# Kernel optimization log

Hardware: AMD Instinct MI355X
Metric: run time of the kernel (lower is better)

Reference implementation:

```python
import jax, jax.numpy as jnp
import numpy as np

N_NODES = 100000
N_EDGES = 800000
NFEAT, NHID, NCLASS = 500, 64, 16


def _spmm(src, dst, edge_w, feat, n_nodes):
    # sparse adj @ feat:  out[i] = sum_{e: dst[e]=i} edge_w[e] * feat[src[e]]
    gathered = edge_w[:, None] * feat[src]  # [E, F]
    return jax.ops.segment_sum(gathered, dst, num_segments=n_nodes)


def setup_inputs() -> dict:
    key = jax.random.key(0)
    ks = jax.random.split(key, 8)
    return {
        "x": jax.random.normal(ks[0], (N_NODES, NFEAT), dtype=jnp.float32),
        "W1": jax.random.normal(ks[1], (NFEAT, NHID), dtype=jnp.float32) / np.sqrt(NFEAT),
        "b1": jax.random.normal(ks[2], (NHID,), dtype=jnp.float32) * 0.01,
        "W2": jax.random.normal(ks[3], (NHID, NCLASS), dtype=jnp.float32) / np.sqrt(NHID),
        "b2": jax.random.normal(ks[4], (NCLASS,), dtype=jnp.float32) * 0.01,
        "edge_w": jax.random.uniform(ks[5], (N_EDGES,), dtype=jnp.float32),
        "src": jax.random.randint(ks[6], (N_EDGES,), 0, N_NODES, dtype=jnp.int32),
        "dst": jax.random.randint(ks[7], (N_EDGES,), 0, N_NODES, dtype=jnp.int32),
    }


def reference(x, W1, b1, W2, b2, edge_w, src, dst):
    n = x.shape[0]
    # Layer 1: GraphConvolution -> ReLU (dropout is identity in eval mode)
    h = jax.nn.relu(_spmm(src, dst, edge_w, x @ W1, n) + b1)
    # Layer 2: GraphConvolution
    out = _spmm(src, dst, edge_w, h @ W2, n) + b2
    return out
```

## Files before the change

kernel.cpp:

```cpp
#include <hip/hip_runtime.h>

#define NN 100000
#define NE 800000
#define NF 500
#define NH 64
#define NC 16
#define SCAN_B 98
#define G1TILES 782
#define ROLEB 224

typedef __attribute__((ext_vector_type(4))) float f32x4;
typedef __attribute__((ext_vector_type(8))) short bf16x8;

__device__ __forceinline__ unsigned int f2bf(float f) {
    union { float f; unsigned int u; } v; v.f = f;
    return (v.u + 0x7FFFu + ((v.u >> 16) & 1u)) >> 16;
}
__device__ __forceinline__ unsigned int pkbf(float a, float b) {
    return f2bf(a) | (f2bf(b) << 16);
}
__device__ __forceinline__ float bfbits_lo(unsigned int u) { return __uint_as_float(u << 16); }
__device__ __forceinline__ float bfbits_hi(unsigned int u) { return __uint_as_float(u & 0xffff0000u); }

#define GLOAD_LDS16(g, l) __builtin_amdgcn_global_load_lds(                      \
    (const __attribute__((address_space(1))) void*)(g),                          \
    (__attribute__((address_space(3))) void*)(l), 16, 0, 0)

__global__ __launch_bounds__(256) void k_zero(int4* __restrict__ p) {
    int i = blockIdx.x * 256 + threadIdx.x;
    if (i < NN / 4) p[i] = make_int4(0, 0, 0, 0);
}

__global__ __launch_bounds__(1024) void k_scanA(const int* __restrict__ deg, int* __restrict__ bsum) {
    __shared__ int s[1024];
    int t = threadIdx.x, i = blockIdx.x * 1024 + t;
    s[t] = (i < NN) ? deg[i] : 0;
    __syncthreads();
    for (int off = 512; off > 0; off >>= 1) {
        if (t < off) s[t] += s[t + off];
        __syncthreads();
    }
    if (t == 0) bsum[blockIdx.x] = s[0];
}

__global__ __launch_bounds__(1024) void k_scanC(const int* __restrict__ deg, const int* __restrict__ bsum,
                                                int* __restrict__ start, int* __restrict__ cursor) {
    __shared__ int s[1024];
    __shared__ int bs[128];
    int t = threadIdx.x, i = blockIdx.x * 1024 + t;
    if (t < 128) bs[t] = (t < SCAN_B) ? bsum[t] : 0;
    int d = (i < NN) ? deg[i] : 0;
    s[t] = d;
    __syncthreads();
    for (int off = 1; off < 128; off <<= 1) {
        int u = 0;
        if (t < 128 && t >= off) u = bs[t - off];
        __syncthreads();
        if (t < 128 && t >= off) bs[t] += u;
        __syncthreads();
    }
    for (int off = 1; off < 1024; off <<= 1) {
        int u = (t >= off) ? s[t - off] : 0;
        __syncthreads();
        s[t] += u;
        __syncthreads();
    }
    int base = (blockIdx.x == 0) ? 0 : bs[blockIdx.x - 1];
    if (i < NN) {
        int ex = base + s[t] - d;
        start[i] = ex;
        cursor[i] = ex;
    }
    if (blockIdx.x == SCAN_B - 1 && t == 0) start[NN] = bs[SCAN_B - 1];
}

__global__ void k_scatter(const int* __restrict__ src, const int* __restrict__ dst,
                          const float* __restrict__ ew, int* __restrict__ cursor,
                          int2* __restrict__ edges) {
    int e = blockIdx.x * 256 + threadIdx.x;
    if (e < NE) {
        int p = atomicAdd(&cursor[dst[e]], 1);
        edges[p] = make_int2(src[e], __float_as_int(ew[e]));
    }
}

__global__ __launch_bounds__(256) void k_g1(const float* __restrict__ x,
                                            const float* __restrict__ W1,
                                            unsigned char* __restrict__ h1f,
                                            const int* __restrict__ dst, int* __restrict__ deg) {
    __shared__ float xs[128 * 64];
    __shared__ unsigned short ws[64 * 64];
    const int bid = blockIdx.x, tid = threadIdx.x;
    if (bid >= G1TILES) {
        int rb = bid - G1TILES;
        for (int e = rb * 256 + tid; e < NE; e += ROLEB * 256)
            atomicAdd(&deg[dst[e]], 1);
        return;
    }
    const int lane = tid & 63;
    const int wv   = tid >> 6;
    const int row0 = bid * 128;

    f32x4 acc[2][4];
#pragma unroll
    for (int i = 0; i < 2; ++i)
#pragma unroll
        for (int j = 0; j < 4; ++j) acc[i][j] = (f32x4){0.f, 0.f, 0.f, 0.f};

    const int lr    = lane >> 4;
    const int lsl   = (lane & 15) >> 1;
    const int lhalf = lane & 1;
    const long maxidx = (long)NN * NF - 4;

    for (int kt = 0; kt < 8; ++kt) {
        const int k0 = kt * 64;
#pragma unroll
        for (int i = 0; i < 8; ++i) {
            int r  = wv * 32 + i * 4 + lr;
            int gm = row0 + r; if (gm >= NN) gm = NN - 1;
            long gi = (long)gm * NF + k0 + ((lsl ^ (r & 7)) << 3) + (lhalf << 2);
            if (gi > maxidx) gi = maxidx;
            GLOAD_LDS16(x + gi, xs + (wv * 32 + i * 4) * 64);
        }
#pragma unroll
        for (int p = 0; p < 2; ++p) {
            int u  = tid + p * 256;
            int n  = u & 63, sl = u >> 6;
            int gk = k0 + sl * 8;
            float e[8];
#pragma unroll
            for (int j = 0; j < 8; ++j)
                e[j] = (gk + j < NF) ? W1[(long)(gk + j) * NH + n] : 0.f;
            uint4 pk;
            pk.x = pkbf(e[0], e[1]);
            pk.y = pkbf(e[2], e[3]);
            pk.z = pkbf(e[4], e[5]);
            pk.w = pkbf(e[6], e[7]);
            *(uint4*)(ws + n * 64 + (sl ^ (n & 7)) * 8) = pk;
        }
        __syncthreads();
#pragma unroll
        for (int ks = 0; ks < 2; ++ks) {
            const int kg = ks * 4 + (lane >> 4);
            bf16x8 af[2], bfr[4];
#pragma unroll
            for (int i = 0; i < 2; ++i) {
                int r = wv * 32 + i * 16 + (lane & 15);
                const float* srcp = xs + r * 64 + ((kg ^ (r & 7)) << 3);
                f32x4 lo = *(const f32x4*)(srcp);
                f32x4 hi = *(const f32x4*)(srcp + 4);
                uint4 pk;
                pk.x = pkbf(lo[0], lo[1]);
                pk.y = pkbf(lo[2], lo[3]);
                pk.z = pkbf(hi[0], hi[1]);
                pk.w = pkbf(hi[2], hi[3]);
                af[i] = *(bf16x8*)&pk;
            }
#pragma unroll
            for (int j = 0; j < 4; ++j) {
                int n = j * 16 + (lane & 15);
                bfr[j] = *(const bf16x8*)(ws + n * 64 + (kg ^ (n & 7)) * 8);
            }
#pragma unroll
            for (int i = 0; i < 2; ++i)
#pragma unroll
                for (int j = 0; j < 4; ++j)
                    acc[i][j] = __builtin_amdgcn_mfma_f32_16x16x32_bf16(af[i], bfr[j], acc[i][j], 0, 0, 0);
        }
        __syncthreads();
    }
    unsigned char* xb = (unsigned char*)xs;
    const int c = lane & 15;
#pragma unroll
    for (int i = 0; i < 2; ++i) {
#pragma unroll
        for (int q = 0; q < 4; ++q) {
            int r = wv * 32 + i * 16 + (lane >> 4) * 4 + q;
            int pk01 = __builtin_amdgcn_cvt_pk_fp8_f32(acc[i][0][q], acc[i][1][q], 0, false);
            int pk23 = __builtin_amdgcn_cvt_pk_fp8_f32(acc[i][2][q], acc[i][3][q], 0, false);
            xb[r * 64 + 0 * 16 + c] = (unsigned char)(pk01 & 0xff);
            xb[r * 64 + 1 * 16 + c] = (unsigned char)((pk01 >> 8) & 0xff);
            xb[r * 64 + 2 * 16 + c] = (unsigned char)(pk23 & 0xff);
            xb[r * 64 + 3 * 16 + c] = (unsigned char)((pk23 >> 8) & 0xff);
        }
    }
    __syncthreads();
    {
        int rr = tid >> 1, off = (tid & 1) * 32;
        int gm = row0 + rr;
        if (gm < NN) {
            uint4 a = *(uint4*)(xb + rr * 64 + off);
            uint4 b = *(uint4*)(xb + rr * 64 + off + 16);
            *(uint4*)(h1f + (long)gm * 64 + off)      = a;
            *(uint4*)(h1f + (long)gm * 64 + off + 16) = b;
        }
    }
}

__global__ __launch_bounds__(256) void k_l1(const int* __restrict__ start,
                                            const int2* __restrict__ edges,
                                            const unsigned char* __restrict__ h1f,
                                            const float* __restrict__ b1,
                                            const float* __restrict__ W2,
                                            unsigned short* __restrict__ h2b) {
    __shared__ float w2s[NH * NC];
    const int tid = threadIdx.x;
    const float4 w2stage = *(const float4*)(W2 + tid * 4);

    const int lane = tid & 63;
    const int wid  = ((blockIdx.x * 256 + tid) >> 6) * 2 + (lane >> 5);
    const int fo   = lane & 7;
    const int es   = (lane >> 3) & 3;

    const int s = start[wid], e = start[wid + 1];
    float a[8] = {0.f, 0.f, 0.f, 0.f, 0.f, 0.f, 0.f, 0.f};
    int p = s + es;
    while (p + 4 < e) {
        const int2 r0 = edges[p];
        const int2 r1 = edges[p + 4];
        const uint2 v0 = *(const uint2*)(h1f + (long)r0.x * 64 + fo * 8);
        const uint2 v1 = *(const uint2*)(h1f + (long)r1.x * 64 + fo * 8);
        const float w0 = __int_as_float(r0.y);
        const float w1 = __int_as_float(r1.y);
        a[0] += w0 * __builtin_amdgcn_cvt_f32_fp8(v0.x, 0);
        a[1] += w0 * __builtin_amdgcn_cvt_f32_fp8(v0.x, 1);
        a[2] += w0 * __builtin_amdgcn_cvt_f32_fp8(v0.x, 2);
        a[3] += w0 * __builtin_amdgcn_cvt_f32_fp8(v0.x, 3);
        a[4] += w0 * __builtin_amdgcn_cvt_f32_fp8(v0.y, 0);
        a[5] += w0 * __builtin_amdgcn_cvt_f32_fp8(v0.y, 1);
        a[6] += w0 * __builtin_amdgcn_cvt_f32_fp8(v0.y, 2);
        a[7] += w0 * __builtin_amdgcn_cvt_f32_fp8(v0.y, 3);
        a[0] += w1 * __builtin_amdgcn_cvt_f32_fp8(v1.x, 0);
        a[1] += w1 * __builtin_amdgcn_cvt_f32_fp8(v1.x, 1);
        a[2] += w1 * __builtin_amdgcn_cvt_f32_fp8(v1.x, 2);
        a[3] += w1 * __builtin_amdgcn_cvt_f32_fp8(v1.x, 3);
        a[4] += w1 * __builtin_amdgcn_cvt_f32_fp8(v1.y, 0);
        a[5] += w1 * __builtin_amdgcn_cvt_f32_fp8(v1.y, 1);
        a[6] += w1 * __builtin_amdgcn_cvt_f32_fp8(v1.y, 2);
        a[7] += w1 * __builtin_amdgcn_cvt_f32_fp8(v1.y, 3);
        p += 8;
    }
    if (p < e) {
        const int2 r0 = edges[p];
        const uint2 v0 = *(const uint2*)(h1f + (long)r0.x * 64 + fo * 8);
        const float w0 = __int_as_float(r0.y);
        a[0] += w0 * __builtin_amdgcn_cvt_f32_fp8(v0.x, 0);
        a[1] += w0 * __builtin_amdgcn_cvt_f32_fp8(v0.x, 1);
        a[2] += w0 * __builtin_amdgcn_cvt_f32_fp8(v0.x, 2);
        a[3] += w0 * __builtin_amdgcn_cvt_f32_fp8(v0.x, 3);
        a[4] += w0 * __builtin_amdgcn_cvt_f32_fp8(v0.y, 0);
        a[5] += w0 * __builtin_amdgcn_cvt_f32_fp8(v0.y, 1);
        a[6] += w0 * __builtin_amdgcn_cvt_f32_fp8(v0.y, 2);
        a[7] += w0 * __builtin_amdgcn_cvt_f32_fp8(v0.y, 3);
    }
    *(float4*)(w2s + tid * 4) = w2stage;
    __syncthreads();
#pragma unroll
    for (int m = 8; m <= 16; m <<= 1)
#pragma unroll
        for (int j = 0; j < 8; ++j) a[j] += __shfl_xor(a[j], m, 64);
    const float4 ba = *(const float4*)(b1 + fo * 8);
    const float4 bb = *(const float4*)(b1 + fo * 8 + 4);
    float r[8];
    r[0] = fmaxf(a[0] + ba.x, 0.f); r[1] = fmaxf(a[1] + ba.y, 0.f);
    r[2] = fmaxf(a[2] + ba.z, 0.f); r[3] = fmaxf(a[3] + ba.w, 0.f);
    r[4] = fmaxf(a[4] + bb.x, 0.f); r[5] = fmaxf(a[5] + bb.y, 0.f);
    r[6] = fmaxf(a[6] + bb.z, 0.f); r[7] = fmaxf(a[7] + bb.w, 0.f);
    float p0 = 0.f, p1 = 0.f, p2 = 0.f, p3 = 0.f;
#pragma unroll
    for (int j = 0; j < 8; ++j) {
        const f32x4 wv = *(const f32x4*)(w2s + (fo * 8 + j) * NC + es * 4);
        p0 += r[j] * wv[0]; p1 += r[j] * wv[1];
        p2 += r[j] * wv[2]; p3 += r[j] * wv[3];
    }
#pragma unroll
    for (int m = 1; m <= 4; m <<= 1) {
        p0 += __shfl_xor(p0, m, 64); p1 += __shfl_xor(p1, m, 64);
        p2 += __shfl_xor(p2, m, 64); p3 += __shfl_xor(p3, m, 64);
    }
    if (fo == 0) {
        uint2 pk;
        pk.x = pkbf(p0, p1);
        pk.y = pkbf(p2, p3);
        *(uint2*)(h2b + (long)wid * NC + es * 4) = pk;
    }
}

__global__ __launch_bounds__(256) void k_spmm2(const int* __restrict__ start,
                                               const int2* __restrict__ edges,
                                               const unsigned short* __restrict__ h2b,
                                               const float* __restrict__ b2,
                                               float* __restrict__ out) {
    const int lane = threadIdx.x & 63;
    const int wid  = ((blockIdx.x * 256 + threadIdx.x) >> 6) * 4 + (lane >> 4);
    const int es   = (lane >> 2) & 3;
    const int f4   = lane & 3;
    const int s = start[wid], e = start[wid + 1];
    float4 acc = make_float4(0.f, 0.f, 0.f, 0.f);
    int p = s + es;
    while (p + 4 < e) {
        const int2 r0 = edges[p];
        const int2 r1 = edges[p + 4];
        const uint2 v0 = *(const uint2*)(h2b + (long)r0.x * NC + f4 * 4);
        const uint2 v1 = *(const uint2*)(h2b + (long)r1.x * NC + f4 * 4);
        const float w0 = __int_as_float(r0.y);
        const float w1 = __int_as_float(r1.y);
        acc.x += w0 * bfbits_lo(v0.x); acc.y += w0 * bfbits_hi(v0.x);
        acc.z += w0 * bfbits_lo(v0.y); acc.w += w0 * bfbits_hi(v0.y);
        acc.x += w1 * bfbits_lo(v1.x); acc.y += w1 * bfbits_hi(v1.x);
        acc.z += w1 * bfbits_lo(v1.y); acc.w += w1 * bfbits_hi(v1.y);
        p += 8;
    }
    if (p < e) {
        const int2 r0 = edges[p];
        const uint2 v0 = *(const uint2*)(h2b + (long)r0.x * NC + f4 * 4);
        const float w0 = __int_as_float(r0.y);
        acc.x += w0 * bfbits_lo(v0.x); acc.y += w0 * bfbits_hi(v0.x);
        acc.z += w0 * bfbits_lo(v0.y); acc.w += w0 * bfbits_hi(v0.y);
    }
#pragma unroll
    for (int m = 4; m <= 8; m <<= 1) {
        acc.x += __shfl_xor(acc.x, m, 64); acc.y += __shfl_xor(acc.y, m, 64);
        acc.z += __shfl_xor(acc.z, m, 64); acc.w += __shfl_xor(acc.w, m, 64);
    }
    if (es == 0) {
        const float4 b = *(const float4*)(b2 + f4 * 4);
        float4 r;
        r.x = acc.x + b.x; r.y = acc.y + b.y;
        r.z = acc.z + b.z; r.w = acc.w + b.w;
        *(float4*)(out + (long)wid * NC + f4 * 4) = r;
    }
}

extern "C" void kernel_launch(void* const* d_in, const int* in_sizes, int n_in,
                              void* d_out, int out_size, void* d_ws, size_t ws_size,
                              hipStream_t stream) {
    const float* x   = (const float*)d_in[0];
    const float* W1  = (const float*)d_in[1];
    const float* b1  = (const float*)d_in[2];
    const float* W2  = (const float*)d_in[3];
    const float* b2  = (const float*)d_in[4];
    const float* ew  = (const float*)d_in[5];
    const int*   src = (const int*)d_in[6];
    const int*   dst = (const int*)d_in[7];
    float* out = (float*)d_out;

    char* w = (char*)d_ws;
    unsigned char*  h1f = (unsigned char*)(w + 0);
    unsigned short* h2b = (unsigned short*)(w + 25600000);
    int*   bsum   = (int*) (w + 32000000);
    int*   startp = (int*) (w + 32001024);
    int*   cursor = (int*) (w + 32402048);
    int2*  edges  = (int2*)(w + 32803072);

    k_zero   <<<(NN / 4 + 255) / 256, 256, 0, stream>>>((int4*)cursor);
    k_g1     <<<G1TILES + ROLEB, 256, 0, stream>>>(x, W1, h1f, dst, cursor);
    k_scanA  <<<SCAN_B, 1024, 0, stream>>>(cursor, bsum);
    k_scanC  <<<SCAN_B, 1024, 0, stream>>>(cursor, bsum, startp, cursor);
    k_scatter<<<(NE + 255) / 256, 256, 0, stream>>>(src, dst, ew, cursor, edges);
    k_l1     <<<(NN / 2 * 64) / 256, 256, 0, stream>>>(startp, edges, h1f, b1, W2, h2b);
    k_spmm2  <<<(NN / 4 * 64) / 256, 256, 0, stream>>>(startp, edges, h2b, b2, out);
}
```

Baseline: 160.7 us.

## Split layer-1 aggregation into two feature-half passes for cache locality

```diff
diff --git a/kernel.cpp b/kernel.cpp
--- a/kernel.cpp
+++ b/kernel.cpp
@@ -86,7 +86,8 @@
 
 __global__ __launch_bounds__(256) void k_g1(const float* __restrict__ x,
                                             const float* __restrict__ W1,
-                                            unsigned char* __restrict__ h1f,
+                                            unsigned char* __restrict__ h1fA,
+                                            unsigned char* __restrict__ h1fB,
                                             const int* __restrict__ dst, int* __restrict__ deg) {
     __shared__ float xs[128 * 64];
     __shared__ unsigned short ws[64 * 64];
@@ -186,40 +187,44 @@
     }
     __syncthreads();
     {
-        int rr = tid >> 1, off = (tid & 1) * 32;
+        int rr = tid >> 1, half = tid & 1;
         int gm = row0 + rr;
         if (gm < NN) {
-            uint4 a = *(uint4*)(xb + rr * 64 + off);
-            uint4 b = *(uint4*)(xb + rr * 64 + off + 16);
-            *(uint4*)(h1f + (long)gm * 64 + off)      = a;
-            *(uint4*)(h1f + (long)gm * 64 + off + 16) = b;
-        }
-    }
-}
-
-__global__ __launch_bounds__(256) void k_l1(const int* __restrict__ start,
-                                            const int2* __restrict__ edges,
-                                            const unsigned char* __restrict__ h1f,
-                                            const float* __restrict__ b1,
-                                            const float* __restrict__ W2,
-                                            unsigned short* __restrict__ h2b) {
-    __shared__ float w2s[NH * NC];
+            unsigned char* dstb = half ? h1fB : h1fA;
+            uint4 a = *(uint4*)(xb + rr * 64 + half * 32);
+            uint4 b = *(uint4*)(xb + rr * 64 + half * 32 + 16);
+            *(uint4*)(dstb + (long)gm * 32)      = a;
+            *(uint4*)(dstb + (long)gm * 32 + 16) = b;
+        }
+    }
+}
+
+template<int PASS_B>
+__global__ __launch_bounds__(256) void k_l1p(const int* __restrict__ start,
+                                             const int2* __restrict__ edges,
+                                             const unsigned char* __restrict__ h1h,
+                                             const float* __restrict__ b1h,
+                                             const float* __restrict__ W2h,
+                                             float* __restrict__ h2p,
+                                             unsigned short* __restrict__ h2b) {
+    __shared__ float w2s[32 * NC];
     const int tid = threadIdx.x;
-    const float4 w2stage = *(const float4*)(W2 + tid * 4);
+    const float2 w2stage = *(const float2*)(W2h + tid * 2);
 
     const int lane = tid & 63;
     const int wid  = ((blockIdx.x * 256 + tid) >> 6) * 2 + (lane >> 5);
-    const int fo   = lane & 7;
-    const int es   = (lane >> 3) & 3;
+    const int w5   = lane & 31;
+    const int fq   = w5 & 3;
+    const int es   = w5 >> 2;
 
     const int s = start[wid], e = start[wid + 1];
     float a[8] = {0.f, 0.f, 0.f, 0.f, 0.f, 0.f, 0.f, 0.f};
     int p = s + es;
-    while (p + 4 < e) {
+    while (p + 8 < e) {
         const int2 r0 = edges[p];
-        const int2 r1 = edges[p + 4];
-        const uint2 v0 = *(const uint2*)(h1f + (long)r0.x * 64 + fo * 8);
-        const uint2 v1 = *(const uint2*)(h1f + (long)r1.x * 64 + fo * 8);
+        const int2 r1 = edges[p + 8];
+        const uint2 v0 = *(const uint2*)(h1h + (long)r0.x * 32 + fq * 8);
+        const uint2 v1 = *(const uint2*)(h1h + (long)r1.x * 32 + fq * 8);
         const float w0 = __int_as_float(r0.y);
         const float w1 = __int_as_float(r1.y);
         a[0] += w0 * __builtin_amdgcn_cvt_f32_fp8(v0.x, 0);
@@ -238,11 +243,11 @@
         a[5] += w1 * __builtin_amdgcn_cvt_f32_fp8(v1.y, 1);
         a[6] += w1 * __builtin_amdgcn_cvt_f32_fp8(v1.y, 2);
         a[7] += w1 * __builtin_amdgcn_cvt_f32_fp8(v1.y, 3);
-        p += 8;
+        p += 16;
     }
     if (p < e) {
         const int2 r0 = edges[p];
-        const uint2 v0 = *(const uint2*)(h1f + (long)r0.x * 64 + fo * 8);
+        const uint2 v0 = *(const uint2*)(h1h + (long)r0.x * 32 + fq * 8);
         const float w0 = __int_as_float(r0.y);
         a[0] += w0 * __builtin_amdgcn_cvt_f32_fp8(v0.x, 0);
         a[1] += w0 * __builtin_amdgcn_cvt_f32_fp8(v0.x, 1);
@@ -253,36 +258,38 @@
         a[6] += w0 * __builtin_amdgcn_cvt_f32_fp8(v0.y, 2);
         a[7] += w0 * __builtin_amdgcn_cvt_f32_fp8(v0.y, 3);
     }
-    *(float4*)(w2s + tid * 4) = w2stage;
+    *(float2*)(w2s + tid * 2) = w2stage;
     __syncthreads();
 #pragma unroll
-    for (int m = 8; m <= 16; m <<= 1)
+    for (int m = 4; m <= 16; m <<= 1)
 #pragma unroll
         for (int j = 0; j < 8; ++j) a[j] += __shfl_xor(a[j], m, 64);
-    const float4 ba = *(const float4*)(b1 + fo * 8);
-    const float4 bb = *(const float4*)(b1 + fo * 8 + 4);
     float r[8];
-    r[0] = fmaxf(a[0] + ba.x, 0.f); r[1] = fmaxf(a[1] + ba.y, 0.f);
-    r[2] = fmaxf(a[2] + ba.z, 0.f); r[3] = fmaxf(a[3] + ba.w, 0.f);
-    r[4] = fmaxf(a[4] + bb.x, 0.f); r[5] = fmaxf(a[5] + bb.y, 0.f);
-    r[6] = fmaxf(a[6] + bb.z, 0.f); r[7] = fmaxf(a[7] + bb.w, 0.f);
+#pragma unroll
+    for (int j = 0; j < 8; ++j) r[j] = fmaxf(a[j] + b1h[fq * 8 + j], 0.f);
+    const int o4 = es & 3;
     float p0 = 0.f, p1 = 0.f, p2 = 0.f, p3 = 0.f;
 #pragma unroll
     for (int j = 0; j < 8; ++j) {
-        const f32x4 wv = *(const f32x4*)(w2s + (fo * 8 + j) * NC + es * 4);
+        const f32x4 wv = *(const f32x4*)(w2s + (fq * 8 + j) * NC + o4 * 4);
         p0 += r[j] * wv[0]; p1 += r[j] * wv[1];
         p2 += r[j] * wv[2]; p3 += r[j] * wv[3];
     }
 #pragma unroll
-    for (int m = 1; m <= 4; m <<= 1) {
+    for (int m = 1; m <= 2; m <<= 1) {
         p0 += __shfl_xor(p0, m, 64); p1 += __shfl_xor(p1, m, 64);
         p2 += __shfl_xor(p2, m, 64); p3 += __shfl_xor(p3, m, 64);
     }
-    if (fo == 0) {
-        uint2 pk;
-        pk.x = pkbf(p0, p1);
-        pk.y = pkbf(p2, p3);
-        *(uint2*)(h2b + (long)wid * NC + es * 4) = pk;
+    if (fq == 0 && es < 4) {
+        if (PASS_B) {
+            const float4 pa = *(const float4*)(h2p + (long)wid * NC + o4 * 4);
+            uint2 pk;
+            pk.x = pkbf(p0 + pa.x, p1 + pa.y);
+            pk.y = pkbf(p2 + pa.z, p3 + pa.w);
+            *(uint2*)(h2b + (long)wid * NC + o4 * 4) = pk;
+        } else {
+            *(float4*)(h2p + (long)wid * NC + o4 * 4) = make_float4(p0, p1, p2, p3);
+        }
     }
 }
 
@@ -346,18 +353,21 @@
     float* out = (float*)d_out;
 
     char* w = (char*)d_ws;
-    unsigned char*  h1f = (unsigned char*)(w + 0);
-    unsigned short* h2b = (unsigned short*)(w + 25600000);
+    unsigned char*  h1fA = (unsigned char*)(w + 0);
+    unsigned char*  h1fB = (unsigned char*)(w + 3200000);
+    float*          h2p  = (float*)(w + 12800000);
+    unsigned short* h2b  = (unsigned short*)(w + 25600000);
     int*   bsum   = (int*) (w + 32000000);
     int*   startp = (int*) (w + 32001024);
     int*   cursor = (int*) (w + 32402048);
     int2*  edges  = (int2*)(w + 32803072);
 
     k_zero   <<<(NN / 4 + 255) / 256, 256, 0, stream>>>((int4*)cursor);
-    k_g1     <<<G1TILES + ROLEB, 256, 0, stream>>>(x, W1, h1f, dst, cursor);
+    k_g1     <<<G1TILES + ROLEB, 256, 0, stream>>>(x, W1, h1fA, h1fB, dst, cursor);
     k_scanA  <<<SCAN_B, 1024, 0, stream>>>(cursor, bsum);
     k_scanC  <<<SCAN_B, 1024, 0, stream>>>(cursor, bsum, startp, cursor);
     k_scatter<<<(NE + 255) / 256, 256, 0, stream>>>(src, dst, ew, cursor, edges);
-    k_l1     <<<(NN / 2 * 64) / 256, 256, 0, stream>>>(startp, edges, h1f, b1, W2, h2b);
+    k_l1p<0> <<<(NN / 2 * 64) / 256, 256, 0, stream>>>(startp, edges, h1fA, b1,      W2,       h2p, h2b);
+    k_l1p<1> <<<(NN / 2 * 64) / 256, 256, 0, stream>>>(startp, edges, h1fB, b1 + 32, W2 + 512, h2p, h2b);
     k_spmm2  <<<(NN / 4 * 64) / 256, 256, 0, stream>>>(startp, edges, h2b, b2, out);
 }
```

Result: slower. 192.1 us (+19.5%).
